# Performance work log

Measured on AMD Instinct MI355X. Metric: run time of the kernel, lower is better.

Reference implementation:

```python
import jax, jax.numpy as jnp
import numpy as np

MARGIN = 0.2  # matches init_kwargs; margin > 0 -> relu hinge branch

N_PARTS, NUM_CLASSES, K_PER_CLASS, D_FEAT = 64, 32, 16, 256


def setup_inputs() -> dict:
    key = jax.random.key(0)
    m = NUM_CLASSES * K_PER_CLASS  # 512
    feature = jax.random.normal(key, (N_PARTS, m, D_FEAT), dtype=jnp.float32)
    # Structured P x K labels: masked_select(...).view(n, m, -1, 1) in the
    # original requires exactly K positives per anchor, so labels must be
    # K samples per class (identical across the part dimension).
    label = jnp.tile(jnp.repeat(jnp.arange(NUM_CLASSES, dtype=jnp.int64), K_PER_CLASS)[None, :], (N_PARTS, 1))
    return {"feature": feature, "label": label, "num_pos": K_PER_CLASS}


def _batch_euc_dist(x):
    # x: [n, m, d] -> dist: [n, m, m]
    x2 = jnp.sum(x * x, axis=2)  # [n, m]
    d2 = x2[:, :, None] + x2[:, None, :] - 2.0 * jnp.einsum('nid,njd->nij', x, x)
    return jnp.sqrt(jax.nn.relu(d2))


def reference(feature, label, num_pos):
    n, m, d = feature.shape
    dist = _batch_euc_dist(feature)  # [n, m, m]
    same = label[:, :, None] == label[:, None, :]  # [n, m, m] bool
    # masked_select preserves flat (row-major) order, so per anchor the
    # selected positives/negatives appear in increasing index order ->
    # stable argsort on the mask reproduces it exactly.
    pos_idx = jnp.argsort(jnp.where(same, 0, 1), axis=-1)[..., :num_pos]        # [n, m, k]
    neg_idx = jnp.argsort(jnp.where(same, 1, 0), axis=-1)[..., :m - num_pos]    # [n, m, m-k]
    hp = jnp.take_along_axis(dist, pos_idx, axis=-1)[:, :, :, None]   # [n, m, k, 1]
    hn = jnp.take_along_axis(dist, neg_idx, axis=-1)[:, :, None, :]   # [n, m, 1, m-k]
    # margin > 0 -> relu hinge (heter/hard/part mining disabled by init flags)
    loss = jax.nn.relu(MARGIN + hp - hn).reshape(n, -1)               # [n, m*k*(m-k)]
    nonzero_num = jnp.sum(loss != 0, axis=1).astype(loss.dtype)       # [n]
    loss_mean = jnp.where(nonzero_num == 0, 0.0,
                          jnp.sum(loss, axis=1) / jnp.maximum(nonzero_num, 1.0))
    return loss_mean.mean(), nonzero_num.mean()
```

## Files before the change

### kernel.cpp

```cpp
#include <hip/hip_runtime.h>
#include <math.h>


#define MARGIN 0.2f
constexpr int NP = 64;
constexpr int M = 512;
constexpr int D = 256;
constexpr int SDS = 17;

typedef __attribute__((ext_vector_type(8))) short bf16x8;
typedef __attribute__((ext_vector_type(4))) float f32x4;
typedef __attribute__((address_space(1))) const unsigned int as1_uint;
typedef __attribute__((address_space(3))) unsigned int as3_uint;

__device__ __forceinline__ unsigned f2bf(float x) {
  unsigned b = __float_as_uint(x);
  return (b + 0x7FFFu + ((b >> 16) & 1u)) >> 16;
}
__device__ __forceinline__ uint4 pack8u(float4 v0, float4 v1) {
  uint4 p;
  p.x = f2bf(v0.x) | (f2bf(v0.y) << 16);
  p.y = f2bf(v0.z) | (f2bf(v0.w) << 16);
  p.z = f2bf(v1.x) | (f2bf(v1.y) << 16);
  p.w = f2bf(v1.z) | (f2bf(v1.w) << 16);
  return p;
}
__device__ __forceinline__ float sq8(float4 v0, float4 v1) {
  return v0.x * v0.x + v0.y * v0.y + v0.z * v0.z + v0.w * v0.w +
         v1.x * v1.x + v1.y * v1.y + v1.z * v1.z + v1.w * v1.w;
}

__global__ __launch_bounds__(256) void convert_kernel(
    const float* __restrict__ feat, unsigned short* __restrict__ fb,
    float* __restrict__ x2g) {
  const int t = threadIdx.x;
  const int R = blockIdx.x * 8 + (t >> 5);
  const int c = t & 31;
  const int r = R & 63;
  const float* src = feat + (size_t)R * D + c * 8;
  float4 v0 = ((const float4*)src)[0], v1 = ((const float4*)src)[1];
  *(uint4*)&fb[((size_t)R * 32 + (c ^ (r & 7))) * 8] = pack8u(v0, v1);
  float ss = sq8(v0, v1);
  ss += __shfl_xor(ss, 16, 32);
  ss += __shfl_xor(ss, 8, 32);
  ss += __shfl_xor(ss, 4, 32);
  ss += __shfl_xor(ss, 2, 32);
  ss += __shfl_xor(ss, 1, 32);
  if (c == 0) x2g[R] = ss;
}

__global__ __launch_bounds__(512, 2) void triplet_kernel(
    const unsigned short* __restrict__ fb, const float* __restrict__ x2g,
    float* __restrict__ psum, float* __restrict__ pcnt) {
  __shared__ unsigned short Bs[64 * 32 * 8];
  __shared__ float sumt[32 * SDS];
  __shared__ float x2s[2][64];
  __shared__ float reds[8], redc[8];

  const int p = blockIdx.x;
  const int q = blockIdx.y;
  const int i0 = q * 32;
  const int T0 = q >> 1;
  const int t = threadIdx.x;
  const int w = t >> 6, L = t & 63;
  const int rw = w & 1;
  const int f = w >> 1;
  const int tx = L & 15, quad = L >> 4;
  const int tx7 = tx & 7;
  const int fp = ((q & 1) << 1) + rw;
  const float* x2p = x2g + (size_t)p * M;

  auto dma_tile = [&](int j0) {
    const char* gsrc = (const char*)fb + ((size_t)p * M + j0) * 512;
    char* lbase = (char*)Bs + w * 1024;
#pragma unroll
    for (int i = 0; i < 4; i++)
      __builtin_amdgcn_global_load_lds((as1_uint*)(gsrc + i * 8192 + t * 16),
                                       (as3_uint*)(lbase + i * 8192), 16, 0, 0);
  };

  dma_tile(T0 * 64);
  if (t < 64) x2s[0][t] = x2p[T0 * 64 + t];

  const size_t Ra = (size_t)p * M + i0 + rw * 16 + tx;
  bf16x8 af[8];
#pragma unroll
  for (int kc = 0; kc < 2; kc++)
#pragma unroll
    for (int ks = 0; ks < 4; ks++) {
      const int ca = kc * 16 + ks * 4 + quad;
      af[kc * 4 + ks] = *(const bf16x8*)&fb[(Ra * 32 + (ca ^ tx7)) * 8];
    }
  const float x2a = x2p[i0 + rw * 16 + tx];

  auto gram = [&](int frag) -> f32x4 {
    f32x4 acc = (f32x4){0.f, 0.f, 0.f, 0.f};
    const int base = (frag * 16 + tx) * 32;
#pragma unroll
    for (int kc = 0; kc < 2; kc++)
#pragma unroll
      for (int ks = 0; ks < 4; ks++) {
        const int cb = kc * 16 + ks * 4 + quad;
        bf16x8 b = *(bf16x8*)&Bs[(base + (cb ^ tx7)) * 8];
        acc = __builtin_amdgcn_mfma_f32_16x16x32_bf16(b, af[kc * 4 + ks], acc,
                                                      0, 0, 0);
      }
    return acc;
  };

  __syncthreads();

  float v[16];
  {
    f32x4 pacc = gram(fp);
    f32x4 x2jp = *(const f32x4*)&x2s[0][fp * 16 + quad * 4];
    float dp0 = MARGIN + sqrtf(fmaxf(x2a + x2jp[0] - 2.f * pacc[0], 0.f));
    float dp1 = MARGIN + sqrtf(fmaxf(x2a + x2jp[1] - 2.f * pacc[1], 0.f));
    float dp2 = MARGIN + sqrtf(fmaxf(x2a + x2jp[2] - 2.f * pacc[2], 0.f));
    float dp3 = MARGIN + sqrtf(fmaxf(x2a + x2jp[3] - 2.f * pacc[3], 0.f));
    v[0] = dp0; v[1] = dp1; v[2] = dp2; v[3] = dp3;
    v[4] = __shfl_xor(dp0, 16, 64);
    v[5] = __shfl_xor(dp1, 16, 64);
    v[6] = __shfl_xor(dp2, 16, 64);
    v[7] = __shfl_xor(dp3, 16, 64);
    v[8] = __shfl_xor(dp0, 32, 64);
    v[9] = __shfl_xor(dp1, 32, 64);
    v[10] = __shfl_xor(dp2, 32, 64);
    v[11] = __shfl_xor(dp3, 32, 64);
    v[12] = __shfl_xor(v[4], 32, 64);
    v[13] = __shfl_xor(v[5], 32, 64);
    v[14] = __shfl_xor(v[6], 32, 64);
    v[15] = __shfl_xor(v[7], 32, 64);
  }

  f32x4 acc = gram(f);

  __syncthreads();

  {
    const int nj0 = ((T0 + 1) & 7) * 64;
    dma_tile(nj0);
    if (t < 64) x2s[1][t] = x2p[nj0 + t];
  }

#pragma unroll
  for (int k = 2; k <= 16; k <<= 1)
#pragma unroll
    for (int j = k >> 1; j > 0; j >>= 1)
#pragma unroll
      for (int i = 0; i < 16; i++) {
        const int l = i ^ j;
        if (l > i) {
          const bool asc = ((i & k) == 0);
          if (asc ? (v[i] > v[l]) : (v[i] < v[l])) {
            float tmp = v[i]; v[i] = v[l]; v[l] = tmp;
          }
        }
      }

  const int sb = (rw * 16 + tx) * SDS;
  if (w < 2 && quad == 0) {
    float run = 0.f;
    sumt[sb + 0] = 0.f;
#pragma unroll
    for (int c = 1; c <= 16; c++) {
      run += v[16 - c];
      sumt[sb + c] = run;
    }
  }

  float hsum = 0.f;
  int hcnt = 0;

  for (int ti = 0; ti < 8; ti++) {
    __syncthreads();
    if (ti > 0) {
      acc = gram(f);
      __syncthreads();
      if (ti < 7) {
        const int nj0 = ((T0 + ti + 1) & 7) * 64;
        dma_tile(nj0);
        if (t < 64) x2s[(ti + 1) & 1][t] = x2p[nj0 + t];
      }
    }

    if (!(ti == 0 && f == fp)) {
      const f32x4 x2j = *(const f32x4*)&x2s[ti & 1][f * 16 + quad * 4];
#pragma unroll
      for (int r = 0; r < 4; r++) {
        const float dn = sqrtf(fmaxf(x2a + x2j[r] - 2.f * acc[r], 0.f));
        int c = 0;
#pragma unroll
        for (int k = 0; k < 16; k++) c += (v[k] > dn) ? 1 : 0;
        hsum += sumt[sb + c];
        hsum = fmaf(-(float)c, dn, hsum);
        hcnt += c;
      }
    }
  }

  float cf = (float)hcnt;
  for (int off = 32; off > 0; off >>= 1) {
    hsum += __shfl_down(hsum, off, 64);
    cf += __shfl_down(cf, off, 64);
  }
  if (L == 0) { reds[w] = hsum; redc[w] = cf; }
  __syncthreads();
  if (t == 0) {
    float bs = 0.f, bc = 0.f;
#pragma unroll
    for (int i = 0; i < 8; i++) { bs += reds[i]; bc += redc[i]; }
    psum[p * 16 + q] = bs;
    pcnt[p * 16 + q] = bc;
  }
}

__global__ __launch_bounds__(64) void finalize_kernel(
    const float* __restrict__ psum, const float* __restrict__ pcnt,
    float* __restrict__ out) {
  const int p = threadIdx.x;
  float s = 0.f, c = 0.f;
#pragma unroll
  for (int i = 0; i < 16; i++) {
    s += psum[p * 16 + i];
    c += pcnt[p * 16 + i];
  }
  float lm = (c == 0.f) ? 0.f : s / fmaxf(c, 1.f);
  float ctot = c;
  for (int off = 32; off > 0; off >>= 1) {
    lm += __shfl_down(lm, off, 64);
    ctot += __shfl_down(ctot, off, 64);
  }
  if (p == 0) {
    out[0] = lm / 64.f;
    out[1] = ctot / 64.f;
  }
}

extern "C" void kernel_launch(void* const* d_in, const int* in_sizes, int n_in,
                              void* d_out, int out_size, void* d_ws,
                              size_t ws_size, hipStream_t stream) {
  const float* feat = (const float*)d_in[0];
  float* ws = (float*)d_ws;
  float* psum = ws;
  float* pcnt = ws + 1024;
  float* x2g = ws + 2048;
  unsigned short* fb = (unsigned short*)(ws + 2048 + 32768);
  float* out = (float*)d_out;

  convert_kernel<<<(NP * M) / 8, 256, 0, stream>>>(feat, fb, x2g);
  dim3 grid(NP, 16);
  triplet_kernel<<<grid, 512, 0, stream>>>(fb, x2g, psum, pcnt);
  finalize_kernel<<<1, 64, 0, stream>>>(psum, pcnt, out);
}
```

Before: 119.3 us.

## Replace linear positive-count scan with branchless binary search on squared distances

The per-negative count of violating positives used to be a 16-way compare loop; it is now a 4-level branchless binary search over the sorted positives, squared so the comparison runs against d² before the sqrt. The prefix-sum table is reindexed as a suffix table and the count is inverted (counting non-violators), with the total recovered from the number of processed elements. It also hoists B-tile LDS offsets out of the gram loop, reuses the positive gram tile when the fragments coincide, and uses a raw v_sqrt_f32 instead of sqrtf. The aim is to cut VALU work in the inner hinge loop, at the cost of exactness differences from the approximate sqrt and from squaring margin-shifted values.

```diff
diff --git a/kernel.cpp b/kernel.cpp
--- a/kernel.cpp
+++ b/kernel.cpp
@@ -6,13 +6,18 @@
 constexpr int NP = 64;
 constexpr int M = 512;
 constexpr int D = 256;
-constexpr int SDS = 17;
+constexpr int TDS = 17;
 
 typedef __attribute__((ext_vector_type(8))) short bf16x8;
 typedef __attribute__((ext_vector_type(4))) float f32x4;
 typedef __attribute__((address_space(1))) const unsigned int as1_uint;
 typedef __attribute__((address_space(3))) unsigned int as3_uint;
 
+__device__ __forceinline__ float fsqrt_fast(float x) {
+  float r;
+  asm("v_sqrt_f32 %0, %1" : "=v"(r) : "v"(x));
+  return r;
+}
 __device__ __forceinline__ unsigned f2bf(float x) {
   unsigned b = __float_as_uint(x);
   return (b + 0x7FFFu + ((b >> 16) & 1u)) >> 16;
@@ -53,7 +58,7 @@
     const unsigned short* __restrict__ fb, const float* __restrict__ x2g,
     float* __restrict__ psum, float* __restrict__ pcnt) {
   __shared__ unsigned short Bs[64 * 32 * 8];
-  __shared__ float sumt[32 * SDS];
+  __shared__ float tab[32 * TDS];
   __shared__ float x2s[2][64];
   __shared__ float reds[8], redc[8];
 
@@ -93,31 +98,36 @@
     }
   const float x2a = x2p[i0 + rw * 16 + tx];
 
+  int boff[8];
+#pragma unroll
+  for (int kc = 0; kc < 2; kc++)
+#pragma unroll
+    for (int ks = 0; ks < 4; ks++) {
+      const int cb = kc * 16 + ks * 4 + quad;
+      boff[kc * 4 + ks] = (tx * 32 + (cb ^ tx7)) * 16;
+    }
+
   auto gram = [&](int frag) -> f32x4 {
     f32x4 acc = (f32x4){0.f, 0.f, 0.f, 0.f};
-    const int base = (frag * 16 + tx) * 32;
-#pragma unroll
-    for (int kc = 0; kc < 2; kc++)
-#pragma unroll
-      for (int ks = 0; ks < 4; ks++) {
-        const int cb = kc * 16 + ks * 4 + quad;
-        bf16x8 b = *(bf16x8*)&Bs[(base + (cb ^ tx7)) * 8];
-        acc = __builtin_amdgcn_mfma_f32_16x16x32_bf16(b, af[kc * 4 + ks], acc,
-                                                      0, 0, 0);
-      }
+    const char* base = (const char*)Bs + frag * 8192;
+#pragma unroll
+    for (int k = 0; k < 8; k++) {
+      bf16x8 b = *(const bf16x8*)(base + boff[k]);
+      acc = __builtin_amdgcn_mfma_f32_16x16x32_bf16(b, af[k], acc, 0, 0, 0);
+    }
     return acc;
   };
 
   __syncthreads();
 
   float v[16];
+  f32x4 pacc = gram(fp);
   {
-    f32x4 pacc = gram(fp);
     f32x4 x2jp = *(const f32x4*)&x2s[0][fp * 16 + quad * 4];
-    float dp0 = MARGIN + sqrtf(fmaxf(x2a + x2jp[0] - 2.f * pacc[0], 0.f));
-    float dp1 = MARGIN + sqrtf(fmaxf(x2a + x2jp[1] - 2.f * pacc[1], 0.f));
-    float dp2 = MARGIN + sqrtf(fmaxf(x2a + x2jp[2] - 2.f * pacc[2], 0.f));
-    float dp3 = MARGIN + sqrtf(fmaxf(x2a + x2jp[3] - 2.f * pacc[3], 0.f));
+    float dp0 = MARGIN + fsqrt_fast(fmaxf(x2a + x2jp[0] - 2.f * pacc[0], 0.f));
+    float dp1 = MARGIN + fsqrt_fast(fmaxf(x2a + x2jp[1] - 2.f * pacc[1], 0.f));
+    float dp2 = MARGIN + fsqrt_fast(fmaxf(x2a + x2jp[2] - 2.f * pacc[2], 0.f));
+    float dp3 = MARGIN + fsqrt_fast(fmaxf(x2a + x2jp[3] - 2.f * pacc[3], 0.f));
     v[0] = dp0; v[1] = dp1; v[2] = dp2; v[3] = dp3;
     v[4] = __shfl_xor(dp0, 16, 64);
     v[5] = __shfl_xor(dp1, 16, 64);
@@ -133,7 +143,8 @@
     v[15] = __shfl_xor(v[7], 32, 64);
   }
 
-  f32x4 acc = gram(f);
+  f32x4 acc;
+  if (f != fp) acc = gram(f); else acc = pacc;
 
   __syncthreads();
 
@@ -158,19 +169,22 @@
         }
       }
 
-  const int sb = (rw * 16 + tx) * SDS;
+  const int sb = (rw * 16 + tx) * TDS;
   if (w < 2 && quad == 0) {
     float run = 0.f;
-    sumt[sb + 0] = 0.f;
-#pragma unroll
-    for (int c = 1; c <= 16; c++) {
-      run += v[16 - c];
-      sumt[sb + c] = run;
-    }
-  }
+    tab[sb + 16] = 0.f;
+#pragma unroll
+    for (int idx = 15; idx >= 0; idx--) {
+      run += v[idx];
+      tab[sb + idx] = run;
+    }
+  }
+
+#pragma unroll
+  for (int k = 0; k < 16; k++) v[k] = v[k] * v[k];
 
   float hsum = 0.f;
-  int hcnt = 0;
+  int scnt = 0;
 
   for (int ti = 0; ti < 8; ti++) {
     __syncthreads();
@@ -188,18 +202,35 @@
       const f32x4 x2j = *(const f32x4*)&x2s[ti & 1][f * 16 + quad * 4];
 #pragma unroll
       for (int r = 0; r < 4; r++) {
-        const float dn = sqrtf(fmaxf(x2a + x2j[r] - 2.f * acc[r], 0.f));
-        int c = 0;
-#pragma unroll
-        for (int k = 0; k < 16; k++) c += (v[k] > dn) ? 1 : 0;
-        hsum += sumt[sb + c];
-        hsum = fmaf(-(float)c, dn, hsum);
-        hcnt += c;
+        const float d2 = fmaxf(fmaf(-2.f, acc[r], x2a + x2j[r]), 0.f);
+        const float dn = fsqrt_fast(d2);
+        const bool b0 = v[7] <= d2;
+        const float p1 = b0 ? v[11] : v[3];
+        const bool b1 = p1 <= d2;
+        const float t0 = b0 ? v[9] : v[1];
+        const float t1 = b0 ? v[13] : v[5];
+        const float p2 = b1 ? t1 : t0;
+        const bool b2 = p2 <= d2;
+        const float a0 = b0 ? v[8] : v[0];
+        const float a1 = b0 ? v[10] : v[2];
+        const float a2 = b0 ? v[12] : v[4];
+        const float a3 = b0 ? v[14] : v[6];
+        const float c0 = b1 ? a2 : a0;
+        const float c1 = b1 ? a3 : a1;
+        const float p3 = b2 ? c1 : c0;
+        const bool b3 = p3 <= d2;
+        int cnt = (b0 ? 8 : 0) | (b1 ? 4 : 0) | (b2 ? 2 : 0) | (b3 ? 1 : 0);
+        cnt += (b0 && b1 && b2 && b3 && (v[15] <= d2)) ? 1 : 0;
+        hsum += tab[sb + cnt];
+        hsum = fmaf((float)cnt - 16.f, dn, hsum);
+        scnt += cnt;
       }
     }
   }
 
-  float cf = (float)hcnt;
+  const int np = (f == fp) ? 28 : 32;
+  float cf = (float)(16 * np - scnt);
+
   for (int off = 32; off > 0; off >>= 1) {
     hsum += __shfl_down(hsum, off, 64);
     cf += __shfl_down(cf, off, 64);
```

Result: faster. 110.6 us (median of 2 runs) (-7.4%).
